# Kernel tuning notes

Measured on AMD Instinct MI355X. Metric: run time of the kernel, lower is better.

Reference implementation:

```python
import jax, jax.numpy as jnp
import numpy as np
import math

HEADS = 16
D = 1024
HEAD_DIM = D // HEADS
SEQ = 2048
BATCH = 4
LN_EPS = 1e-5


def setup_inputs() -> dict:
    key = jax.random.key(0)
    ks = jax.random.split(key, 7)
    s = 1.0 / math.sqrt(HEAD_DIM)
    return {
        "q": jax.random.normal(ks[0], (SEQ, BATCH, D), dtype=jnp.float32),
        "k": jax.random.normal(ks[1], (SEQ, BATCH, D), dtype=jnp.float32),
        "v": jax.random.normal(ks[2], (SEQ, BATCH, D), dtype=jnp.float32),
        "Wq": jax.random.normal(ks[3], (HEAD_DIM, HEAD_DIM), dtype=jnp.float32) * s,
        "Wk": jax.random.normal(ks[4], (HEAD_DIM, HEAD_DIM), dtype=jnp.float32) * s,
        "Wv": jax.random.normal(ks[5], (HEAD_DIM, HEAD_DIM), dtype=jnp.float32) * s,
        "Wl": jax.random.normal(ks[6], (D, D), dtype=jnp.float32) * (1.0 / math.sqrt(D)),
        "gamma": jnp.ones((D,), dtype=jnp.float32),
        "beta": jnp.zeros((D,), dtype=jnp.float32),
    }


def reference(q, k, v, Wq, Wk, Wv, Wl, gamma, beta):
    # q, k, v: [seq_len, batch, d]  (seq-first, as in the torch module)
    q_len, batch = q.shape[0], q.shape[1]
    k_len, v_len = k.shape[0], v.shape[0]
    # Faithful to torch: reshape (NOT transpose) seq-first tensor into
    # (batch, len, heads, head_dim), then per-head linear (x @ W.T, no bias).
    Qh = jnp.einsum('bqhd,ed->bqhe', q.reshape(batch, q_len, HEADS, HEAD_DIM), Wq)
    Kh = jnp.einsum('bkhd,ed->bkhe', k.reshape(batch, k_len, HEADS, HEAD_DIM), Wk)
    Vh = jnp.einsum('bvhd,ed->bvhe', v.reshape(batch, v_len, HEADS, HEAD_DIM), Wv)
    # Scores scaled by sqrt(d) (full model dim), as in the original.
    scores = jnp.einsum('bqhd,bkhd->bhqk', Qh, Kh) / math.sqrt(D)
    attn = jax.nn.softmax(scores, axis=-1)  # dropout p=0.0 -> identity
    out = jnp.einsum('bhqk,bkhd->bqhd', attn, Vh)  # [b, q, h, d]
    concat = out.reshape(q_len, batch, D)
    lin = concat @ Wl.T
    mean = jnp.mean(lin, axis=-1, keepdims=True)
    var = jnp.var(lin, axis=-1, keepdims=True)
    ln = (lin - mean) * jax.lax.rsqrt(var + LN_EPS) * gamma + beta
    return q + ln
```

## Files before the change

### kernel.cpp

```cpp
#include <hip/hip_runtime.h>

#define LOG2E 1.4426950408889634f

typedef __attribute__((ext_vector_type(8))) short short8_t;
typedef __attribute__((ext_vector_type(4))) float floatx4;
typedef __attribute__((ext_vector_type(16))) float floatx16;

#define MFMA(a,b,c)   __builtin_amdgcn_mfma_f32_16x16x32_bf16(a,b,c,0,0,0)
#define MFMA32(a,b,c) __builtin_amdgcn_mfma_f32_32x32x16_bf16(a,b,c,0,0,0)
#define GLOAD(g, l) __builtin_amdgcn_global_load_lds( \
    (const __attribute__((address_space(1))) unsigned int*)(g), \
    (__attribute__((address_space(3))) unsigned int*)(l), 16, 0, 0)

__device__ __forceinline__ unsigned short f2bf(float f){
    unsigned u = __float_as_uint(f);
    u = u + 0x7FFFu + ((u >> 16) & 1u);
    return (unsigned short)(u >> 16);
}
__device__ __forceinline__ float bf2f(unsigned short s){
    return __uint_as_float(((unsigned)s) << 16);
}
__device__ __forceinline__ unsigned cvtpk(float lo, float hi){
    unsigned r;
    asm("v_cvt_pk_bf16_f32 %0, %1, %2" : "=v"(r) : "v"(lo), "v"(hi));
    return r;
}
__device__ __forceinline__ void plswap(unsigned &a, unsigned &b){
    asm volatile("v_permlane32_swap_b32 %0, %1" : "+v"(a), "+v"(b));
}

union U8 { unsigned u[4]; short8_t s8; };

__global__ __launch_bounds__(256) void proj_kernel(
    const float* __restrict__ Xq, const float* __restrict__ Xk, const float* __restrict__ Xv,
    const float* __restrict__ Wq, const float* __restrict__ Wk, const float* __restrict__ Wv,
    unsigned short* __restrict__ qp, unsigned short* __restrict__ kp, unsigned short* __restrict__ vp)
{
    const int rt = blockIdx.x;
    const int h  = blockIdx.y;
    const int sel= blockIdx.z;
    const float* X = (sel==0)?Xq:(sel==1)?Xk:Xv;
    const float* W = (sel==0)?Wq:(sel==1)?Wk:Wv;
    unsigned short* O = (sel==0)?qp:(sel==1)?kp:vp;
    const float qs = (sel==0) ? ((1.0f/32.0f)*LOG2E) : 1.0f;

    const int t  = threadIdx.x;
    const int w  = t >> 6, l = t & 63;
    const int r5 = l & 31;
    const int hf = l >> 5;

    const int row0 = rt*128 + w*32;

    short8_t a[4];
    {
        const float* xb = X + (size_t)(row0 + r5)*1024 + h*64 + hf*8;
        #pragma unroll
        for (int kb=0; kb<4; kb++){
            float4 f0 = *reinterpret_cast<const float4*>(xb + kb*16);
            float4 f1 = *reinterpret_cast<const float4*>(xb + kb*16 + 4);
            U8 u;
            u.u[0] = cvtpk(f0.x, f0.y); u.u[1] = cvtpk(f0.z, f0.w);
            u.u[2] = cvtpk(f1.x, f1.y); u.u[3] = cvtpk(f1.z, f1.w);
            a[kb] = u.s8;
        }
    }
    short8_t b[2][4];
    #pragma unroll
    for (int nb=0; nb<2; nb++){
        const float* wb = W + (size_t)(nb*32 + r5)*64 + hf*8;
        #pragma unroll
        for (int kb=0; kb<4; kb++){
            float4 f0 = *reinterpret_cast<const float4*>(wb + kb*16);
            float4 f1 = *reinterpret_cast<const float4*>(wb + kb*16 + 4);
            U8 u;
            u.u[0] = cvtpk(f0.x, f0.y); u.u[1] = cvtpk(f0.z, f0.w);
            u.u[2] = cvtpk(f1.x, f1.y); u.u[3] = cvtpk(f1.z, f1.w);
            b[nb][kb] = u.s8;
        }
    }

    floatx16 acc[2] = {};
    #pragma unroll
    for (int nb=0; nb<2; nb++)
        #pragma unroll
        for (int kb=0; kb<4; kb++)
            acc[nb] = MFMA32(a[kb], b[nb][kb], acc[nb]);

    const int c   = rt >> 4;
    const size_t chbase = (size_t)(c*16 + h);

    #pragma unroll
    for (int nb=0; nb<2; nb++){
        const int e = nb*32 + r5;
        #pragma unroll
        for (int m=0; m<4; m++){
            unsigned p01 = cvtpk(acc[nb][4*m]*qs,   acc[nb][4*m+1]*qs);
            unsigned p23 = cvtpk(acc[nb][4*m+2]*qs, acc[nb][4*m+3]*qs);
            #pragma unroll
            for (int i=0; i<4; i++){
                unsigned short val = (unsigned short)
                    ((i==0)?p01 : (i==1)?(p01>>16) : (i==2)?p23 : (p23>>16));
                const int gr = row0 + i + 8*m + 4*hf;
                const int s  = gr & 2047;
                size_t addr;
                if (sel == 0){
                    addr = (chbase*2048 + s)*64 + e;
                } else {
                    const int kt_ = s >> 6, rl = s & 63;
                    const size_t tbase = (chbase*32 + kt_)*4096;
                    if (sel == 1)
                        addr = tbase + rl*64 + (((e>>3) ^ (rl&7))<<3) + (e&7);
                    else
                        addr = tbase + e*64 + (((rl>>3) ^ (e&7))<<3) + (rl&7);
                }
                O[addr] = val;
            }
        }
    }
}

__global__ __launch_bounds__(256,1) void attn_kernel(
    const unsigned short* __restrict__ qp, const unsigned short* __restrict__ kp,
    const unsigned short* __restrict__ vp, unsigned short* __restrict__ ob)
{
    const int bswz = blockIdx.x;
    const int xr   = bswz & 7;
    const int rest = bswz >> 3;
    const int qt   = rest & 15;
    const int p    = xr + 8*(rest >> 4);
    const int hd   = p & 15;
    const int c    = p >> 4;

    const int t  = threadIdx.x;
    const int w  = t >> 6, l = t & 63;
    const int r5 = l & 31;
    const int hf = l >> 5;

    __shared__ unsigned short Ks[2][64][64];
    __shared__ unsigned short Vs[2][64][64];

    const size_t chq = ((size_t)(c*16 + hd))*2048*64;
    const size_t cht = ((size_t)(c*16 + hd))*32*4096;

    short8_t aq[4];
    {
        const unsigned short* qrow = qp + chq + (size_t)(qt*128 + w*32 + r5)*64 + hf*8;
        #pragma unroll
        for (int kb=0;kb<4;kb++)
            aq[kb] = *reinterpret_cast<const short8_t*>(qrow + kb*16);
    }

    const char* kbase = (const char*)(kp + cht) + w*2048 + l*16;
    const char* vbase = (const char*)(vp + cht) + w*2048 + l*16;
    char* kdst = (char*)(&Ks[0][0][0]) + w*2048;
    char* vdst = (char*)(&Vs[0][0][0]) + w*2048;

    #define ATTN_STAGE(buf, kt) do { \
        const char* ks_ = kbase + (size_t)(kt)*8192; \
        const char* vs_ = vbase + (size_t)(kt)*8192; \
        char* kd_ = kdst + (buf)*8192; \
        char* vd_ = vdst + (buf)*8192; \
        GLOAD(ks_,      kd_);      GLOAD(ks_+1024, kd_+1024); \
        GLOAD(vs_,      vd_);      GLOAD(vs_+1024, vd_+1024); \
    } while(0)

    const int x7 = r5 & 7;

    U8 onesu;
    onesu.u[0] = 0x3F803F80u; onesu.u[1] = 0x3F803F80u;
    onesu.u[2] = 0x3F803F80u; onesu.u[3] = 0x3F803F80u;
    const short8_t ones8 = onesu.s8;

    floatx16 oa[2] = {};
    floatx16 lsv = {};

    ATTN_STAGE(0, 0);

    for (int kt=0; kt<32; kt++){
        const int cur = kt & 1;
        if (kt < 31){
            ATTN_STAGE(cur^1, kt+1);
            asm volatile("s_waitcnt vmcnt(4)" ::: "memory");
        } else {
            asm volatile("s_waitcnt vmcnt(0)" ::: "memory");
        }
        __builtin_amdgcn_s_barrier();
        __builtin_amdgcn_sched_barrier(0);

        const unsigned short* Kc = &Ks[cur][0][0];
        const unsigned short* Vc = &Vs[cur][0][0];

        floatx16 sacc[2] = {};
        __builtin_amdgcn_s_setprio(1);
        #pragma unroll
        for (int mb=0;mb<2;mb++){
            #pragma unroll
            for (int kb=0;kb<4;kb++){
                short8_t kf = *reinterpret_cast<const short8_t*>(
                    Kc + (mb*32 + r5)*64 + (((kb*2 + hf) ^ x7)<<3));
                sacc[mb] = MFMA32(kf, aq[kb], sacc[mb]);
            }
        }
        __builtin_amdgcn_s_setprio(0);

        #pragma unroll
        for (int mb=0;mb<2;mb++)
            #pragma unroll
            for (int i=0;i<16;i++)
                sacc[mb][i] = __builtin_amdgcn_exp2f(sacc[mb][i]);

        short8_t F[4];
        #pragma unroll
        for (int mb=0;mb<2;mb++){
            unsigned lo[4], hi[4];
            #pragma unroll
            for (int m=0;m<4;m++){
                lo[m] = cvtpk(sacc[mb][4*m],   sacc[mb][4*m+1]);
                hi[m] = cvtpk(sacc[mb][4*m+2], sacc[mb][4*m+3]);
            }
            #pragma unroll
            for (int hk=0;hk<2;hk++){
                unsigned a = lo[2*hk], b = lo[2*hk+1];
                unsigned cc = hi[2*hk], d = hi[2*hk+1];
                plswap(a, b);
                plswap(cc, d);
                U8 fu;
                fu.u[0] = a; fu.u[1] = cc; fu.u[2] = b; fu.u[3] = d;
                F[mb*2 + hk] = fu.s8;
            }
        }

        __builtin_amdgcn_s_setprio(1);
        #pragma unroll
        for (int f=0;f<4;f++) lsv = MFMA32(ones8, F[f], lsv);
        #pragma unroll
        for (int db=0;db<2;db++){
            #pragma unroll
            for (int kb2=0;kb2<4;kb2++){
                short8_t vf = *reinterpret_cast<const short8_t*>(
                    Vc + (db*32 + r5)*64 + (((kb2*2 + hf) ^ x7)<<3));
                oa[db] = MFMA32(vf, F[kb2], oa[db]);
            }
        }
        __builtin_amdgcn_s_setprio(0);

        __builtin_amdgcn_sched_barrier(0);
        __builtin_amdgcn_s_barrier();
    }

    const float inv = 1.0f / lsv[0];
    const size_t grow = (size_t)c*2048 + qt*128 + w*32 + r5;
    unsigned short* obp = ob + grow*1024 + hd*64 + hf*4;
    #pragma unroll
    for (int db=0;db<2;db++){
        #pragma unroll
        for (int m=0;m<4;m++){
            ushort4 u;
            u.x = f2bf(oa[db][4*m]*inv);   u.y = f2bf(oa[db][4*m+1]*inv);
            u.z = f2bf(oa[db][4*m+2]*inv); u.w = f2bf(oa[db][4*m+3]*inv);
            *reinterpret_cast<ushort4*>(obp + db*32 + m*8) = u;
        }
    }
}

__global__ __launch_bounds__(256) void wlconv_kernel(const float* __restrict__ W,
                                                     unsigned short* __restrict__ O)
{
    int i = (blockIdx.x*256 + threadIdx.x)*4;
    float4 f = *reinterpret_cast<const float4*>(W + i);
    ushort4 u;
    u.x = f2bf(f.x); u.y = f2bf(f.y); u.z = f2bf(f.z); u.w = f2bf(f.w);
    *reinterpret_cast<ushort4*>(O + i) = u;
}

__global__ __launch_bounds__(256) void gemm_kernel(
    const unsigned short* __restrict__ A, const unsigned short* __restrict__ B,
    unsigned short* __restrict__ C)
{
    const int bm = blockIdx.x, bn = blockIdx.y;
    __shared__ unsigned short As[2][128][64];
    __shared__ unsigned short Bs[2][128][64];
    const int t = threadIdx.x, w = t>>6, l = t&63;
    const int l15 = l&15, l4 = l>>4;
    const int wm = w>>1, wn = w&1;

    const char* asrc = (const char*)A + ((size_t)(bm*128 + w*32 + (l>>3)))*2048 + (l&7)*16;
    const char* bsrc = (const char*)B + ((size_t)(bn*128 + w*32 + (l>>3)))*2048 + (l&7)*16;
    char* adst = (char*)(&As[0][0][0]) + w*4096;
    char* bdst = (char*)(&Bs[0][0][0]) + w*4096;

    #define GEMM_STAGE(buf, kt) do { \
        const char* as_ = asrc + (size_t)(kt)*128; \
        const char* bs_ = bsrc + (size_t)(kt)*128; \
        char* ad_ = adst + (buf)*16384; \
        char* bd_ = bdst + (buf)*16384; \
        GLOAD(as_,          ad_);        GLOAD(as_+16384,  ad_+1024); \
        GLOAD(as_+32768,    ad_+2048);   GLOAD(as_+49152,  ad_+3072); \
        GLOAD(bs_,          bd_);        GLOAD(bs_+16384,  bd_+1024); \
        GLOAD(bs_+32768,    bd_+2048);   GLOAD(bs_+49152,  bd_+3072); \
    } while(0)

    floatx4 acc[4][4] = {};

    GEMM_STAGE(0, 0);

    for (int kt=0; kt<16; kt++){
        const int cur = kt & 1;
        if (kt < 15){
            GEMM_STAGE(cur^1, kt+1);
            asm volatile("s_waitcnt vmcnt(8)" ::: "memory");
        } else {
            asm volatile("s_waitcnt vmcnt(0)" ::: "memory");
        }
        __builtin_amdgcn_s_barrier();
        __builtin_amdgcn_sched_barrier(0);

        #pragma unroll
        for (int kk=0;kk<2;kk++){
            short8_t a[4], b[4];
            #pragma unroll
            for (int mt=0;mt<4;mt++)
                a[mt] = *reinterpret_cast<const short8_t*>(&As[cur][wm*64 + mt*16 + l15][kk*32 + l4*8]);
            #pragma unroll
            for (int nt=0;nt<4;nt++)
                b[nt] = *reinterpret_cast<const short8_t*>(&Bs[cur][wn*64 + nt*16 + l15][kk*32 + l4*8]);
            __builtin_amdgcn_s_setprio(1);
            #pragma unroll
            for (int mt=0;mt<4;mt++)
                #pragma unroll
                for (int nt=0;nt<4;nt++)
                    acc[mt][nt] = MFMA(a[mt], b[nt], acc[mt][nt]);
            __builtin_amdgcn_s_setprio(0);
        }

        __builtin_amdgcn_sched_barrier(0);
        __builtin_amdgcn_s_barrier();
    }

    #pragma unroll
    for (int mt=0;mt<4;mt++)
        #pragma unroll
        for (int nt=0;nt<4;nt++)
            #pragma unroll
            for (int j=0;j<4;j++){
                int row = bm*128 + wm*64 + mt*16 + l4*4 + j;
                int col = bn*128 + wn*64 + nt*16 + l15;
                C[(size_t)row*1024 + col] = f2bf(acc[mt][nt][j]);
            }
}

__global__ __launch_bounds__(256) void ln_kernel(
    const unsigned short* __restrict__ lin, const float* __restrict__ qin,
    const float* __restrict__ gamma, const float* __restrict__ beta, float* __restrict__ out)
{
    const int r = blockIdx.x, t = threadIdx.x;
    const unsigned short* row = lin + (size_t)r*1024;
    uint2 u = *reinterpret_cast<const uint2*>(row + t*4);
    float v0 = bf2f((unsigned short)(u.x & 0xffffu));
    float v1 = bf2f((unsigned short)(u.x >> 16));
    float v2 = bf2f((unsigned short)(u.y & 0xffffu));
    float v3 = bf2f((unsigned short)(u.y >> 16));
    float s  = v0+v1+v2+v3;
    float sq = v0*v0+v1*v1+v2*v2+v3*v3;
    #pragma unroll
    for (int d=1; d<64; d<<=1){ s += __shfl_xor(s, d); sq += __shfl_xor(sq, d); }
    __shared__ float red[8];
    if ((t&63)==0){ red[(t>>6)*2] = s; red[(t>>6)*2+1] = sq; }
    __syncthreads();
    s  = red[0]+red[2]+red[4]+red[6];
    sq = red[1]+red[3]+red[5]+red[7];
    float mean = s*(1.f/1024.f);
    float var  = sq*(1.f/1024.f) - mean*mean;
    float rs   = rsqrtf(var + 1e-5f);
    int base = r*1024 + t*4;
    float4 qv = *reinterpret_cast<const float4*>(qin + base);
    float4 g  = *reinterpret_cast<const float4*>(gamma + t*4);
    float4 b  = *reinterpret_cast<const float4*>(beta + t*4);
    float4 o;
    o.x = qv.x + (v0-mean)*rs*g.x + b.x;
    o.y = qv.y + (v1-mean)*rs*g.y + b.y;
    o.z = qv.z + (v2-mean)*rs*g.z + b.z;
    o.w = qv.w + (v3-mean)*rs*g.w + b.w;
    *reinterpret_cast<float4*>(out + base) = o;
}

extern "C" void kernel_launch(void* const* d_in, const int* in_sizes, int n_in,
                              void* d_out, int out_size, void* d_ws, size_t ws_size,
                              hipStream_t stream)
{
    (void)in_sizes; (void)n_in; (void)out_size; (void)ws_size;
    const float* q     = (const float*)d_in[0];
    const float* k     = (const float*)d_in[1];
    const float* v     = (const float*)d_in[2];
    const float* Wq    = (const float*)d_in[3];
    const float* Wk    = (const float*)d_in[4];
    const float* Wv    = (const float*)d_in[5];
    const float* Wl    = (const float*)d_in[6];
    const float* gamma = (const float*)d_in[7];
    const float* beta  = (const float*)d_in[8];
    float* out = (float*)d_out;

    char* ws = (char*)d_ws;
    unsigned short* qp  = (unsigned short*)(ws);
    unsigned short* kp  = (unsigned short*)(ws + (16u<<20));
    unsigned short* vp  = (unsigned short*)(ws + (32u<<20));
    unsigned short* ob  = (unsigned short*)(ws + (48u<<20));
    unsigned short* lin = (unsigned short*)(ws);
    unsigned short* wlb = (unsigned short*)(ws + (16u<<20));

    proj_kernel <<<dim3(64,16,3),  256, 0, stream>>>(q,k,v, Wq,Wk,Wv, qp,kp,vp);
    attn_kernel <<<dim3(1024),     256, 0, stream>>>(qp,kp,vp, ob);
    wlconv_kernel<<<dim3(1024),    256, 0, stream>>>(Wl, wlb);
    gemm_kernel <<<dim3(64,8),     256, 0, stream>>>(ob, wlb, lin);
    ln_kernel   <<<dim3(8192),     256, 0, stream>>>(lin, q, gamma, beta, out);
}
```

Before: 185.8 us.

## Software-pipeline attention loop: overlap previous PV MFMAs with current exp/softmax

Restructures the attention inner loop into a software pipeline. Each iteration now runs the QK MFMAs for tile kt alongside the PV and row-sum MFMAs for tile kt-1, so matrix work can overlap the exp and bf16-pack VALU work. LDS goes from double to triple buffering, so a single barrier per iteration is enough and the next tile's load is issued after that barrier. The wait becomes vmcnt(0), meaning the prefetch has only one iteration to land. LDS use grows and register pressure rises because the packed probabilities are carried across iterations.

```diff
diff --git a/kernel.cpp b/kernel.cpp
--- a/kernel.cpp
+++ b/kernel.cpp
@@ -136,8 +136,8 @@
     const int r5 = l & 31;
     const int hf = l >> 5;
 
-    __shared__ unsigned short Ks[2][64][64];
-    __shared__ unsigned short Vs[2][64][64];
+    __shared__ unsigned short Ks[3][64][64];
+    __shared__ unsigned short Vs[3][64][64];
 
     const size_t chq = ((size_t)(c*16 + hd))*2048*64;
     const size_t cht = ((size_t)(c*16 + hd))*32*4096;
@@ -152,14 +152,14 @@
 
     const char* kbase = (const char*)(kp + cht) + w*2048 + l*16;
     const char* vbase = (const char*)(vp + cht) + w*2048 + l*16;
-    char* kdst = (char*)(&Ks[0][0][0]) + w*2048;
-    char* vdst = (char*)(&Vs[0][0][0]) + w*2048;
+    char* kdst0 = (char*)(&Ks[0][0][0]) + w*2048;
+    char* vdst0 = (char*)(&Vs[0][0][0]) + w*2048;
 
     #define ATTN_STAGE(buf, kt) do { \
         const char* ks_ = kbase + (size_t)(kt)*8192; \
         const char* vs_ = vbase + (size_t)(kt)*8192; \
-        char* kd_ = kdst + (buf)*8192; \
-        char* vd_ = vdst + (buf)*8192; \
+        char* kd_ = kdst0 + (buf)*8192; \
+        char* vd_ = vdst0 + (buf)*8192; \
         GLOAD(ks_,      kd_);      GLOAD(ks_+1024, kd_+1024); \
         GLOAD(vs_,      vd_);      GLOAD(vs_+1024, vd_+1024); \
     } while(0)
@@ -173,22 +173,23 @@
 
     floatx16 oa[2] = {};
     floatx16 lsv = {};
+    short8_t Fp[4];
 
     ATTN_STAGE(0, 0);
 
+    int cur = 0;
     for (int kt=0; kt<32; kt++){
-        const int cur = kt & 1;
-        if (kt < 31){
-            ATTN_STAGE(cur^1, kt+1);
-            asm volatile("s_waitcnt vmcnt(4)" ::: "memory");
-        } else {
-            asm volatile("s_waitcnt vmcnt(0)" ::: "memory");
-        }
+        const int nxt = (cur==2) ? 0 : cur+1;
+        const int prv = (cur==0) ? 2 : cur-1;
+
+        asm volatile("s_waitcnt vmcnt(0)" ::: "memory");
         __builtin_amdgcn_s_barrier();
         __builtin_amdgcn_sched_barrier(0);
 
+        if (kt < 31) ATTN_STAGE(nxt, kt+1);
+
         const unsigned short* Kc = &Ks[cur][0][0];
-        const unsigned short* Vc = &Vs[cur][0][0];
+        const unsigned short* Vp = &Vs[prv][0][0];
 
         floatx16 sacc[2] = {};
         __builtin_amdgcn_s_setprio(1);
@@ -201,6 +202,19 @@
                 sacc[mb] = MFMA32(kf, aq[kb], sacc[mb]);
             }
         }
+        if (kt > 0){
+            #pragma unroll
+            for (int db=0;db<2;db++){
+                #pragma unroll
+                for (int kb2=0;kb2<4;kb2++){
+                    short8_t vf = *reinterpret_cast<const short8_t*>(
+                        Vp + (db*32 + r5)*64 + (((kb2*2 + hf) ^ x7)<<3));
+                    oa[db] = MFMA32(vf, Fp[kb2], oa[db]);
+                }
+            }
+            #pragma unroll
+            for (int f=0;f<4;f++) lsv = MFMA32(ones8, Fp[f], lsv);
+        }
         __builtin_amdgcn_s_setprio(0);
 
         #pragma unroll
@@ -209,7 +223,6 @@
             for (int i=0;i<16;i++)
                 sacc[mb][i] = __builtin_amdgcn_exp2f(sacc[mb][i]);
 
-        short8_t F[4];
         #pragma unroll
         for (int mb=0;mb<2;mb++){
             unsigned lo[4], hi[4];
@@ -226,26 +239,27 @@
                 plswap(cc, d);
                 U8 fu;
                 fu.u[0] = a; fu.u[1] = cc; fu.u[2] = b; fu.u[3] = d;
-                F[mb*2 + hk] = fu.s8;
-            }
-        }
-
-        __builtin_amdgcn_s_setprio(1);
-        #pragma unroll
-        for (int f=0;f<4;f++) lsv = MFMA32(ones8, F[f], lsv);
+                Fp[mb*2 + hk] = fu.s8;
+            }
+        }
+
+        cur = nxt;
+    }
+
+    {
+        const int prv = (cur==0) ? 2 : cur-1;
+        const unsigned short* Vp = &Vs[prv][0][0];
         #pragma unroll
         for (int db=0;db<2;db++){
             #pragma unroll
             for (int kb2=0;kb2<4;kb2++){
                 short8_t vf = *reinterpret_cast<const short8_t*>(
-                    Vc + (db*32 + r5)*64 + (((kb2*2 + hf) ^ x7)<<3));
-                oa[db] = MFMA32(vf, F[kb2], oa[db]);
-            }
-        }
-        __builtin_amdgcn_s_setprio(0);
-
-        __builtin_amdgcn_sched_barrier(0);
-        __builtin_amdgcn_s_barrier();
+                    Vp + (db*32 + r5)*64 + (((kb2*2 + hf) ^ x7)<<3));
+                oa[db] = MFMA32(vf, Fp[kb2], oa[db]);
+            }
+        }
+        #pragma unroll
+        for (int f=0;f<4;f++) lsv = MFMA32(ones8, Fp[f], lsv);
     }
 
     const float inv = 1.0f / lsv[0];
```

Result: no change. 182.9 us (-1.6%).
